# Optimization experiments

Hardware: AMD Instinct MI355X
Metric: run time of the kernel (lower is better)

Reference implementation:

```python
import jax, jax.numpy as jnp
import numpy as np

NS, B, T, S, H, V, G = 30, 16, 8, 400, 400, 20000, 3


def setup_inputs() -> dict:
    key = jax.random.key(0)
    ks = jax.random.split(key, 16)
    f = lambda k, shp, s: jax.random.normal(k, shp, jnp.float32) * s
    return dict(
        encoded_hidden=f(ks[0], (B, H), 1.0),
        encoded_outputs=f(ks[1], (B, S, H), 1.0),
        slot_emb=f(ks[2], (NS, H), 0.1),
        emb=f(ks[3], (V, H), 0.1),
        W_ih=f(ks[4], (3 * H, H), 0.05),
        W_hh=f(ks[5], (3 * H, H), 0.05),
        b_ih=jnp.zeros((3 * H,), jnp.float32),
        b_hh=jnp.zeros((3 * H,), jnp.float32),
        W_ratio_w=f(ks[6], (1, 3 * H), 0.05),
        W_ratio_b=jnp.zeros((1,), jnp.float32),
        W_gate_w=f(ks[7], (G, H), 0.05),
        W_gate_b=jnp.zeros((G,), jnp.float32),
        story=jax.random.randint(ks[8], (B, S), 0, V),
        target=jax.random.randint(ks[9], (B, NS, T), 0, V),
        encoded_lens=jax.random.randint(ks[10], (B,), S // 2, S + 1).astype(jnp.int32),
    )


def reference(encoded_hidden, encoded_outputs, slot_emb, emb, W_ih, W_hh, b_ih, b_hh,
              W_ratio_w, W_ratio_b, W_gate_w, W_gate_b, story, target, encoded_lens):
    ns, h = slot_emb.shape
    b, s, _ = encoded_outputs.shape
    t = target.shape[2]
    v = emb.shape[0]
    bs = ns * b  # fused slot*batch decode rows (parallel_decode)

    enc_out = jnp.tile(encoded_outputs, (ns, 1, 1))            # [bs,S,H]
    story_r = jnp.tile(story, (ns, 1))                          # [bs,S]
    lens_r = jnp.tile(encoded_lens, (ns,))                      # [bs]
    mask = jnp.arange(s)[None, :] < lens_r[:, None]             # [bs,S]
    h0 = jnp.tile(encoded_hidden, (ns, 1))                      # [bs,H]
    x0 = jnp.broadcast_to(slot_emb[:, None, :], (ns, b, h)).reshape(bs, h)
    # teacher-forcing inputs, slot-major flatten like target[:, :, wi].T.flatten()
    tf_in = emb[jnp.transpose(target, (2, 1, 0)).reshape(t, bs)]  # [T,bs,H]
    row = jnp.arange(bs)[:, None]
    neg_inf = jnp.float32(-jnp.inf)

    def gru_cell(x, hid):
        gi = x @ W_ih.T + b_ih
        gh = hid @ W_hh.T + b_hh
        ir, iz, inn = jnp.split(gi, 3, axis=-1)
        hr, hz, hn = jnp.split(gh, 3, axis=-1)
        r = jax.nn.sigmoid(ir + hr)
        z = jax.nn.sigmoid(iz + hz)
        n = jnp.tanh(inn + r * hn)
        return (1.0 - z) * n + z * hid

    def step(carry, x_next):
        hid, x = carry
        h_new = gru_cell(x, hid)                                # dec_state == hidden for 1-step GRU
        scores = jnp.einsum('bh,bsh->bs', h_new, enc_out)
        scores = jnp.where(mask, scores, neg_inf)
        prob = jax.nn.softmax(scores, axis=1)
        context = jnp.einsum('bs,bsh->bh', prob, enc_out)
        p_vocab = jax.nn.softmax(h_new @ emb.T, axis=1)         # [bs,V]
        p_gen_vec = jnp.concatenate([h_new, context, x], axis=-1)
        switch = jax.nn.sigmoid(p_gen_vec @ W_ratio_w.T + W_ratio_b)  # [bs,1]
        p_ctx = jnp.zeros((bs, v), p_vocab.dtype).at[row, story_r].add(prob)
        final = (1.0 - switch) * p_ctx + switch * p_vocab
        gate = context @ W_gate_w.T + W_gate_b
        return (h_new, x_next), (final, gate)

    _, (finals, gates) = jax.lax.scan(step, (h0, x0), tf_in)
    all_point = finals.reshape(t, ns, b, v).transpose(1, 2, 0, 3)  # [NS,B,T,V]
    all_gate = gates[0].reshape(ns, b, -1)                          # gates from wi==0
    return all_point, all_gate
```

## Files before the change

kernel.cpp:

```cpp
#include <hip/hip_runtime.h>
#include <hip/hip_bf16.h>

#define NSLOT 30
#define BB    16
#define TT    8
#define SS    400
#define HH    400
#define KP    416
#define NKK   13
#define VV    20000
#define GG    3
#define BSR   480
#define NBN   157
#define NCT   1256
#define NG2   1200
#define NCT2  75
#define NRT   30
#define FRAG_STRIDE 512

typedef unsigned short u16;
typedef __attribute__((ext_vector_type(8))) short bf16x8;
typedef __attribute__((ext_vector_type(4))) float f32x4;

__device__ __forceinline__ short f2bfs(float f){
  __hip_bfloat16 h = __float2bfloat16(f);
  union { __hip_bfloat16 b; short u; } v; v.b = h; return v.u;
}
__device__ __forceinline__ unsigned int pack2(float lo, float hi){
  return (unsigned int)(u16)f2bfs(lo) | ((unsigned int)(u16)f2bfs(hi) << 16);
}
__device__ __forceinline__ float bfu(u16 u){
  union { unsigned int i; float f; } v; v.i = ((unsigned int)u) << 16; return v.f;
}
__device__ __forceinline__ float bfu_lo(unsigned int u){
  union { unsigned int i; float f; } v; v.i = u << 16; return v.f;
}
__device__ __forceinline__ float bfu_hi(unsigned int u){
  union { unsigned int i; float f; } v; v.i = u & 0xffff0000u; return v.f;
}
__device__ __forceinline__ float sigm(float x){ return 1.f / (1.f + __expf(-x)); }
__device__ __forceinline__ float tanh_fast(float x){
  float e = __expf(2.f * x);
  return 1.f - 2.f / (e + 1.f);
}
__device__ __forceinline__ float wred_max(float v){
  #pragma unroll
  for (int off = 32; off; off >>= 1) v = fmaxf(v, __shfl_xor(v, off, 64));
  return v;
}
__device__ __forceinline__ float wred_sum(float v){
  #pragma unroll
  for (int off = 32; off; off >>= 1) v += __shfl_xor(v, off, 64);
  return v;
}

__global__ __launch_bounds__(256) void k_init_all(
    const float* __restrict__ eh, const float* __restrict__ semb,
    float* __restrict__ h_ws, float* __restrict__ x_ws,
    short* __restrict__ h_hi, short* __restrict__ h_lo,
    short* __restrict__ x_hi, short* __restrict__ x_lo)
{
  const int NU = NRT * NKK * 64;
  for (int u = blockIdx.x * 256 + threadIdx.x; u < 2 * NU; u += gridDim.x * 256){
    int uu = u; int sel = 0;
    if (uu >= NU){ uu -= NU; sel = 1; }
    short* ph = sel ? x_hi : h_hi;
    short* pl = sel ? x_lo : h_lo;
    float* fw = sel ? x_ws : h_ws;
    int lane = uu & 63, kt = uu >> 6;
    int rtile = kt / NKK, kk = kt - rtile * NKK;
    int lg = lane >> 4, rl = lane & 15;
    int r = rtile * 16 + rl, k = kk * 32 + lg * 8;
    const float* src = sel ? (semb + (size_t)rtile * HH)
                           : (eh   + (size_t)rl * HH);
    bf16x8 oh, ol;
    #pragma unroll
    for (int j = 0; j < 8; ++j){
      if (k + j < HH){
        float v = src[k + j];
        short hb = f2bfs(v);
        oh[j] = hb; ol[j] = f2bfs(v - bfu((u16)hb));
        fw[(size_t)r * HH + k + j] = v;
      } else { oh[j] = 0; ol[j] = 0; }
    }
    *reinterpret_cast<bf16x8*>(ph + (size_t)uu * 8) = oh;
    *reinterpret_cast<bf16x8*>(pl + (size_t)uu * 8) = ol;
  }
}

__global__ __launch_bounds__(256) void k_cast_W(
    const float* __restrict__ Wih, const float* __restrict__ Whh,
    short* __restrict__ Wih_hi, short* __restrict__ Wih_lo,
    short* __restrict__ Whh_hi, short* __restrict__ Whh_lo)
{
  const int NU = NCT2 * NKK * 64;
  for (int u = blockIdx.x * 256 + threadIdx.x; u < 2 * NU; u += gridDim.x * 256){
    int uu = u; int sel = 0;
    if (uu >= NU){ uu -= NU; sel = 1; }
    const float* W = sel ? Whh : Wih;
    short* ph = sel ? Whh_hi : Wih_hi;
    short* pl = sel ? Whh_lo : Wih_lo;
    int lane = uu & 63, kt = uu >> 6;
    int ctile = kt / NKK, kk = kt - ctile * NKK;
    int lg = lane >> 4, cl = lane & 15;
    int c = ctile * 16 + cl, k = kk * 32 + lg * 8;
    bf16x8 oh, ol;
    #pragma unroll
    for (int j = 0; j < 8; ++j){
      if (k + j < HH){
        float v = W[(size_t)c * HH + k + j];
        short hb = f2bfs(v);
        oh[j] = hb; ol[j] = f2bfs(v - bfu((u16)hb));
      } else { oh[j] = 0; ol[j] = 0; }
    }
    *reinterpret_cast<bf16x8*>(ph + (size_t)uu * 8) = oh;
    *reinterpret_cast<bf16x8*>(pl + (size_t)uu * 8) = ol;
  }
}

__global__ __launch_bounds__(256) void k_cast_emb(const float* __restrict__ emb,
                                                  short* __restrict__ ebf)
{
  const int nunit = NCT * NKK * 64;
  for (int u = blockIdx.x * 256 + threadIdx.x; u < nunit; u += gridDim.x * 256){
    int lane = u & 63;
    int kt = u >> 6;
    int ctile = kt / NKK, kk = kt - ctile * NKK;
    int lg = lane >> 4, cl = lane & 15;
    int c = ctile * 16 + cl;
    int k = kk * 32 + lg * 8;
    bf16x8 o;
    if (c < VV && k < HH){
      const float* src = emb + (size_t)c * HH + k;
      #pragma unroll
      for (int j = 0; j < 8; ++j) o[j] = f2bfs(src[j]);
    } else {
      #pragma unroll
      for (int j = 0; j < 8; ++j) o[j] = 0;
    }
    *reinterpret_cast<bf16x8*>(ebf + (size_t)u * 8) = o;
  }
}

__device__ __forceinline__ void gemm2_body(
    int bM, int bN, int z, int t,
    const short* __restrict__ x_hi, const short* __restrict__ x_lo,
    const short* __restrict__ h_hi, const short* __restrict__ h_lo,
    const short* __restrict__ Wih_hi, const short* __restrict__ Wih_lo,
    const short* __restrict__ Whh_hi, const short* __restrict__ Whh_lo,
    float* __restrict__ gi, float* __restrict__ gh)
{
  const int lane = t & 63, wid = t >> 6;
  const int wr = wid >> 1, wc = wid & 1;
  const int l15 = lane & 15, lg = lane >> 4;

  const short* A_hi = z ? h_hi : x_hi;
  const short* A_lo = z ? h_lo : x_lo;
  const short* B_hi = z ? Whh_hi : Wih_hi;
  const short* B_lo = z ? Whh_lo : Wih_lo;
  float* C = z ? gh : gi;

  const short *ah[4], *al[4], *bh[4], *bl[4];
  #pragma unroll
  for (int m = 0; m < 4; ++m){
    int rtile = min(bM * 8 + wr * 4 + m, NRT - 1);
    size_t off = (size_t)rtile * (NKK * FRAG_STRIDE) + lane * 8;
    ah[m] = A_hi + off; al[m] = A_lo + off;
  }
  #pragma unroll
  for (int n = 0; n < 4; ++n){
    int ctile = min(bN * 8 + wc * 4 + n, NCT2 - 1);
    size_t off = (size_t)ctile * (NKK * FRAG_STRIDE) + lane * 8;
    bh[n] = B_hi + off; bl[n] = B_lo + off;
  }

  f32x4 acc[4][4];
  #pragma unroll
  for (int m = 0; m < 4; ++m)
    #pragma unroll
    for (int n = 0; n < 4; ++n)
      acc[m][n] = (f32x4){0.f, 0.f, 0.f, 0.f};

  #pragma unroll
  for (int kk = 0; kk < NKK; ++kk){
    const int ko = kk * FRAG_STRIDE;
    bf16x8 ah_r[4], al_r[4];
    #pragma unroll
    for (int m = 0; m < 4; ++m){
      ah_r[m] = *reinterpret_cast<const bf16x8*>(ah[m] + ko);
      al_r[m] = *reinterpret_cast<const bf16x8*>(al[m] + ko);
    }
    #pragma unroll
    for (int n = 0; n < 4; ++n){
      bf16x8 bhv = *reinterpret_cast<const bf16x8*>(bh[n] + ko);
      bf16x8 blv = *reinterpret_cast<const bf16x8*>(bl[n] + ko);
      #pragma unroll
      for (int m = 0; m < 4; ++m){
        acc[m][n] = __builtin_amdgcn_mfma_f32_16x16x32_bf16(ah_r[m], bhv, acc[m][n], 0, 0, 0);
        acc[m][n] = __builtin_amdgcn_mfma_f32_16x16x32_bf16(ah_r[m], blv, acc[m][n], 0, 0, 0);
        acc[m][n] = __builtin_amdgcn_mfma_f32_16x16x32_bf16(al_r[m], bhv, acc[m][n], 0, 0, 0);
      }
    }
  }

  #pragma unroll
  for (int m = 0; m < 4; ++m){
    #pragma unroll
    for (int q = 0; q < 4; ++q){
      int row = bM * 128 + wr * 64 + m * 16 + lg * 4 + q;
      if (row < BSR){
        #pragma unroll
        for (int n = 0; n < 4; ++n){
          int col = bN * 128 + wc * 64 + n * 16 + l15;
          if (col < NG2) C[(size_t)row * NG2 + col] = acc[m][n][q];
        }
      }
    }
  }
}

__global__ __launch_bounds__(256) void k_gemm2_mfma(
    const short* __restrict__ x_hi, const short* __restrict__ x_lo,
    const short* __restrict__ h_hi, const short* __restrict__ h_lo,
    const short* __restrict__ Wih_hi, const short* __restrict__ Wih_lo,
    const short* __restrict__ Whh_hi, const short* __restrict__ Whh_lo,
    float* __restrict__ gi, float* __restrict__ gh)
{
  gemm2_body(blockIdx.x, blockIdx.y, blockIdx.z, threadIdx.x,
             x_hi, x_lo, h_hi, h_lo, Wih_hi, Wih_lo, Whh_hi, Whh_lo, gi, gh);
}

__global__ __launch_bounds__(256) void k_logits_mfma(
    const short* __restrict__ hbf, const short* __restrict__ ebf,
    float* __restrict__ out, float* __restrict__ pmax_ws,
    float* __restrict__ psum_ws, int wi)
{
  const int t = threadIdx.x;
  const int lane = t & 63, wid = t >> 6;
  const int wr = wid >> 1, wc = wid & 1;
  const int l15 = lane & 15, lg = lane >> 4;
  const int bM = blockIdx.x, bN = blockIdx.y;

  const short* ap[4];
  const short* bp[4];
  #pragma unroll
  for (int m = 0; m < 4; ++m){
    int rtile = bM * 8 + wr * 4 + m;
    ap[m] = hbf + (size_t)min(rtile, NRT - 1) * (NKK * FRAG_STRIDE) + lane * 8;
  }
  #pragma unroll
  for (int n = 0; n < 4; ++n){
    int ctile = bN * 8 + wc * 4 + n;
    bp[n] = ebf + (size_t)ctile * (NKK * FRAG_STRIDE) + lane * 8;
  }

  f32x4 acc[4][4];
  #pragma unroll
  for (int m = 0; m < 4; ++m)
    #pragma unroll
    for (int n = 0; n < 4; ++n)
      acc[m][n] = (f32x4){0.f, 0.f, 0.f, 0.f};

  #pragma unroll
  for (int kk = 0; kk < NKK; ++kk){
    const int ko = kk * FRAG_STRIDE;
    bf16x8 a[4];
    #pragma unroll
    for (int m = 0; m < 4; ++m)
      a[m] = *reinterpret_cast<const bf16x8*>(ap[m] + ko);
    #pragma unroll
    for (int n = 0; n < 4; ++n){
      bf16x8 b = *reinterpret_cast<const bf16x8*>(bp[n] + ko);
      #pragma unroll
      for (int m = 0; m < 4; ++m)
        acc[m][n] = __builtin_amdgcn_mfma_f32_16x16x32_bf16(a[m], b, acc[m][n], 0, 0, 0);
    }
  }

  #pragma unroll
  for (int m = 0; m < 4; ++m){
    #pragma unroll
    for (int q = 0; q < 4; ++q){
      int row = bM * 128 + wr * 64 + m * 16 + lg * 4 + q;
      u16* lrow16 = reinterpret_cast<u16*>(out + ((size_t)row * TT + wi) * VV);
      #pragma unroll
      for (int n = 0; n < 4; ++n){
        float v = acc[m][n][q];
        float vp = __shfl_xor(v, 1, 64);
        int col = bN * 128 + wc * 64 + n * 16 + l15;
        if (((l15 & 1) == 0) && row < BSR && col < VV)
          *reinterpret_cast<unsigned int*>(lrow16 + col) = pack2(v, vp);
      }
    }
    f32x4 rmax, rsum;
    #pragma unroll
    for (int q = 0; q < 4; ++q){
      float mx = -3.0e38f;
      #pragma unroll
      for (int n = 0; n < 4; ++n){
        int col = bN * 128 + wc * 64 + n * 16 + l15;
        float v = (col < VV) ? acc[m][n][q] : -3.0e38f;
        mx = fmaxf(mx, v);
      }
      #pragma unroll
      for (int off = 1; off < 16; off <<= 1) mx = fmaxf(mx, __shfl_xor(mx, off, 64));
      float sm = 0.f;
      #pragma unroll
      for (int n = 0; n < 4; ++n){
        int col = bN * 128 + wc * 64 + n * 16 + l15;
        if (col < VV) sm += __expf(acc[m][n][q] - mx);
      }
      #pragma unroll
      for (int off = 1; off < 16; off <<= 1) sm += __shfl_xor(sm, off, 64);
      rmax[q] = mx; rsum[q] = sm;
    }
    if (l15 == 0){
      #pragma unroll
      for (int q = 0; q < 4; ++q){
        int row = bM * 128 + wr * 64 + m * 16 + lg * 4 + q;
        if (row < BSR){
          size_t pidx = ((size_t)row * NBN + bN) * 2 + wc;
          pmax_ws[pidx] = rmax[q];
          psum_ws[pidx] = rsum[q];
        }
      }
    }
  }
}

__global__ __launch_bounds__(256) void k_att(
    const float* __restrict__ enc, const float* __restrict__ emb,
    const float* __restrict__ b_ih, const float* __restrict__ b_hh,
    const float* __restrict__ Wr_w, const float* __restrict__ Wr_b,
    const float* __restrict__ Wg_w, const float* __restrict__ Wg_b,
    const int* __restrict__ target, const int* __restrict__ lens,
    const float* __restrict__ gi_ws, const float* __restrict__ gh_ws,
    float* __restrict__ h_ws, float* __restrict__ x_ws,
    short* __restrict__ h_hi, short* __restrict__ h_lo,
    short* __restrict__ x_hi, short* __restrict__ x_lo,
    float* __restrict__ prob_ws, float* __restrict__ sw_ws,
    float* __restrict__ d_out, int wi)
{
  __shared__ float hn_s[HH];
  __shared__ float sc_s[SS];
  __shared__ float ctx_s[HH];
  __shared__ float red[4];
  __shared__ float redg[GG][4];

  const int t = threadIdx.x;
  const int rg = blockIdx.x;
  const int batch = rg % BB, slot = rg / BB;
  const int len = lens[batch];
  const int rtile = rg >> 4, rl = rg & 15;

  const float* gir = gi_ws + (size_t)rg * NG2;
  const float* ghr = gh_ws + (size_t)rg * NG2;
  for (int k = t; k < HH; k += 256){
    float irv = gir[k]          + b_ih[k];
    float izv = gir[HH + k]     + b_ih[HH + k];
    float inv = gir[2 * HH + k] + b_ih[2 * HH + k];
    float hrv = ghr[k]          + b_hh[k];
    float hzv = ghr[HH + k]     + b_hh[HH + k];
    float hnv = ghr[2 * HH + k] + b_hh[2 * HH + k];
    float rr = sigm(irv + hrv);
    float zz = sigm(izv + hzv);
    float nn = tanh_fast(inv + rr * hnv);
    float hold = h_ws[(size_t)rg * HH + k];
    float hnew = (1.f - zz) * nn + zz * hold;
    hn_s[k] = hnew;
    h_ws[(size_t)rg * HH + k] = hnew;
  }
  __syncthreads();

  if (t < KP / 8){
    const int kk = t >> 2, lg = t & 3;
    bf16x8 oh, ol;
    #pragma unroll
    for (int j = 0; j < 8; ++j){
      int k = t * 8 + j;
      if (k < HH){
        float v = hn_s[k];
        short hb = f2bfs(v);
        oh[j] = hb; ol[j] = f2bfs(v - bfu((u16)hb));
      } else { oh[j] = 0; ol[j] = 0; }
    }
    size_t off = ((size_t)rtile * NKK + kk) * FRAG_STRIDE + (lg * 16 + rl) * 8;
    *reinterpret_cast<bf16x8*>(h_hi + off) = oh;
    *reinterpret_cast<bf16x8*>(h_lo + off) = ol;
  }

  const float* encb = enc + (size_t)batch * SS * HH;
  float lmax = -3.0e38f;
  for (int s = t; s < SS; s += 256){
    if (s < len){
      const float4* er4 = reinterpret_cast<const float4*>(encb + (size_t)s * HH);
      float dot = 0.f;
      for (int k4 = 0; k4 < HH / 4; ++k4){
        float4 e = er4[k4];
        float4 hv = *reinterpret_cast<const float4*>(&hn_s[k4 * 4]);
        dot += e.x*hv.x + e.y*hv.y + e.z*hv.z + e.w*hv.w;
      }
      sc_s[s] = dot;
      lmax = fmaxf(lmax, dot);
    }
  }
  lmax = wred_max(lmax);
  if ((t & 63) == 0) red[t >> 6] = lmax;
  __syncthreads();
  lmax = fmaxf(fmaxf(red[0], red[1]), fmaxf(red[2], red[3]));
  float lsum = 0.f;
  for (int s = t; s < SS; s += 256){
    float e = (s < len) ? __expf(sc_s[s] - lmax) : 0.f;
    sc_s[s] = e;
    lsum += e;
  }
  lsum = wred_sum(lsum);
  __syncthreads();
  if ((t & 63) == 0) red[t >> 6] = lsum;
  __syncthreads();
  lsum = red[0] + red[1] + red[2] + red[3];
  float invl = 1.f / lsum;
  for (int s = t; s < SS; s += 256){
    float p = sc_s[s] * invl;
    sc_s[s] = p;
    prob_ws[(size_t)rg * SS + s] = p;
  }
  __syncthreads();

  for (int k = t; k < HH; k += 256){
    float c0 = 0.f, c1 = 0.f, c2 = 0.f, c3 = 0.f;
    const float* ek = encb + k;
    int s = 0;
    for (; s + 3 < len; s += 4){
      c0 += sc_s[s]     * ek[(size_t)s * HH];
      c1 += sc_s[s + 1] * ek[(size_t)(s + 1) * HH];
      c2 += sc_s[s + 2] * ek[(size_t)(s + 2) * HH];
      c3 += sc_s[s + 3] * ek[(size_t)(s + 3) * HH];
    }
    for (; s < len; ++s) c0 += sc_s[s] * ek[(size_t)s * HH];
    ctx_s[k] = (c0 + c1) + (c2 + c3);
  }
  __syncthreads();

  float sa = 0.f;
  for (int k = t; k < HH; k += 256){
    sa += Wr_w[k]          * hn_s[k]
        + Wr_w[HH + k]     * ctx_s[k]
        + Wr_w[2 * HH + k] * x_ws[(size_t)rg * HH + k];
  }
  sa = wred_sum(sa);
  if ((t & 63) == 0) red[t >> 6] = sa;
  __syncthreads();
  sa = red[0] + red[1] + red[2] + red[3];
  if (t == 0) sw_ws[rg] = sigm(sa + Wr_b[0]);

  if (wi == 0){
    float ga[GG] = {0.f, 0.f, 0.f};
    for (int k = t; k < HH; k += 256){
      float cv = ctx_s[k];
      ga[0] += Wg_w[k] * cv;
      ga[1] += Wg_w[HH + k] * cv;
      ga[2] += Wg_w[2 * HH + k] * cv;
    }
    #pragma unroll
    for (int g = 0; g < GG; ++g){
      ga[g] = wred_sum(ga[g]);
      if ((t & 63) == 0) redg[g][t >> 6] = ga[g];
    }
    __syncthreads();
    if (t < GG)
      d_out[(size_t)NSLOT * BB * TT * VV + (size_t)rg * GG + t] =
          redg[t][0] + redg[t][1] + redg[t][2] + redg[t][3] + Wg_b[t];
  }

  const int tgt = target[batch * (NSLOT * TT) + slot * TT + wi];
  const float* embrow = emb + (size_t)tgt * HH;
  for (int k = t; k < HH; k += 256)
    x_ws[(size_t)rg * HH + k] = embrow[k];
  if (t < KP / 8){
    const int kk = t >> 2, lg = t & 3;
    bf16x8 oh, ol;
    #pragma unroll
    for (int j = 0; j < 8; ++j){
      int k = t * 8 + j;
      if (k < HH){
        float v = embrow[k];
        short hb = f2bfs(v);
        oh[j] = hb; ol[j] = f2bfs(v - bfu((u16)hb));
      } else { oh[j] = 0; ol[j] = 0; }
    }
    size_t off = ((size_t)rtile * NKK + kk) * FRAG_STRIDE + (lg * 16 + rl) * 8;
    *reinterpret_cast<bf16x8*>(x_hi + off) = oh;
    *reinterpret_cast<bf16x8*>(x_lo + off) = ol;
  }
}

__global__ __launch_bounds__(256) void k_fin_gemm2(
    float* __restrict__ logits_out, const float* __restrict__ prob_ws,
    const float* __restrict__ pmax_ws, const float* __restrict__ psum_ws,
    const float* __restrict__ sw_ws, const int* __restrict__ story,
    const int* __restrict__ lens, int wi,
    const short* __restrict__ x_hi, const short* __restrict__ x_lo,
    const short* __restrict__ h_hi, const short* __restrict__ h_lo,
    const short* __restrict__ Wih_hi, const short* __restrict__ Wih_lo,
    const short* __restrict__ Whh_hi, const short* __restrict__ Whh_lo,
    float* __restrict__ gi, float* __restrict__ gh, int do_gemm)
{
  __shared__ float pctx[VV];
  __shared__ float red[4];
  const int t = threadIdx.x;

  if (blockIdx.x >= BSR){
    if (!do_gemm) return;
    int b = blockIdx.x - BSR;
    int bM = b & 3, bN = (b >> 2) % 10, z = b / 40;
    gemm2_body(bM, bN, z, t, x_hi, x_lo, h_hi, h_lo,
               Wih_hi, Wih_lo, Whh_hi, Whh_lo, gi, gh);
    return;
  }

  const int r = blockIdx.x;
  const int batch = r % BB;
  for (int v = t; v < VV; v += 256) pctx[v] = 0.f;
  __syncthreads();
  const int len = lens[batch];
  for (int s = t; s < SS; s += 256){
    if (s < len)
      atomicAdd(&pctx[story[batch * SS + s]], prob_ws[(size_t)r * SS + s]);
  }

  float* lrow = logits_out + ((size_t)r * TT + wi) * VV;
  const uint4* l16 = reinterpret_cast<const uint4*>(lrow);
  uint4 stage[10];
  {
    int ns = 0;
    for (int i = t; i < VV / 8; i += 256) stage[ns++] = l16[i];
  }

  const float* pm = pmax_ws + (size_t)r * (NBN * 2);
  const float* ps = psum_ws + (size_t)r * (NBN * 2);
  float m = -3.0e38f;
  for (int i = t; i < NBN * 2; i += 256) m = fmaxf(m, pm[i]);
  m = wred_max(m);
  if ((t & 63) == 0) red[t >> 6] = m;
  __syncthreads();
  m = fmaxf(fmaxf(red[0], red[1]), fmaxf(red[2], red[3]));
  float lsum = 0.f;
  for (int i = t; i < NBN * 2; i += 256) lsum += ps[i] * __expf(pm[i] - m);
  lsum = wred_sum(lsum);
  __syncthreads();
  if ((t & 63) == 0) red[t >> 6] = lsum;
  __syncthreads();
  lsum = red[0] + red[1] + red[2] + red[3];

  const float sw = sw_ws[r];
  const float invl = sw / lsum;
  const float osw = 1.f - sw;
  {
    int ns = 0;
    for (int i = t; i < VV / 8; i += 256){
      uint4 q = stage[ns++];
      int v = i * 8;
      float4 o0, o1;
      o0.x = __expf(bfu_lo(q.x) - m) * invl + osw * pctx[v + 0];
      o0.y = __expf(bfu_hi(q.x) - m) * invl + osw * pctx[v + 1];
      o0.z = __expf(bfu_lo(q.y) - m) * invl + osw * pctx[v + 2];
      o0.w = __expf(bfu_hi(q.y) - m) * invl + osw * pctx[v + 3];
      o1.x = __expf(bfu_lo(q.z) - m) * invl + osw * pctx[v + 4];
      o1.y = __expf(bfu_hi(q.z) - m) * invl + osw * pctx[v + 5];
      o1.z = __expf(bfu_lo(q.w) - m) * invl + osw * pctx[v + 6];
      o1.w = __expf(bfu_hi(q.w) - m) * invl + osw * pctx[v + 7];
      *reinterpret_cast<float4*>(lrow + v)     = o0;
      *reinterpret_cast<float4*>(lrow + v + 4) = o1;
    }
  }
}

extern "C" void kernel_launch(void* const* d_in, const int* in_sizes, int n_in,
                              void* d_out, int out_size, void* d_ws, size_t ws_size,
                              hipStream_t stream)
{
  (void)in_sizes; (void)n_in; (void)out_size; (void)ws_size;
  const float* eh    = (const float*)d_in[0];
  const float* enc   = (const float*)d_in[1];
  const float* semb  = (const float*)d_in[2];
  const float* emb   = (const float*)d_in[3];
  const float* W_ih  = (const float*)d_in[4];
  const float* W_hh  = (const float*)d_in[5];
  const float* b_ih  = (const float*)d_in[6];
  const float* b_hh  = (const float*)d_in[7];
  const float* Wr_w  = (const float*)d_in[8];
  const float* Wr_b  = (const float*)d_in[9];
  const float* Wg_w  = (const float*)d_in[10];
  const float* Wg_b  = (const float*)d_in[11];
  const int* story = (const int*)d_in[12];
  const int* tgt   = (const int*)d_in[13];
  const int* lens  = (const int*)d_in[14];
  float* out = (float*)d_out;

  float* ws      = (float*)d_ws;
  float* h_ws    = ws;
  float* x_ws    = ws + 192000;
  float* prob_ws = ws + 384000;
  float* sw_ws   = ws + 576000;
  float* gi_ws   = ws + 576512;
  float* gh_ws   = ws + 1152512;
  float* pmax_ws = ws + 1728512;
  float* psum_ws = ws + 1879552;
  short* h_hi    = (short*)(ws + 2030592);
  short* emb_bf  = (short*)(ws + 2130432);
  short* Wih_hi  = (short*)(ws + 6310400);
  short* Wih_lo  = (short*)(ws + 6560000);
  short* Whh_hi  = (short*)(ws + 6809600);
  short* Whh_lo  = (short*)(ws + 7059200);
  short* x_hi    = (short*)(ws + 7308800);
  short* x_lo    = (short*)(ws + 7408640);
  short* h_lo    = (short*)(ws + 7508480);

  k_cast_emb<<<2048, 256, 0, stream>>>(emb, emb_bf);
  k_cast_W<<<512, 256, 0, stream>>>(W_ih, W_hh, Wih_hi, Wih_lo, Whh_hi, Whh_lo);
  k_init_all<<<195, 256, 0, stream>>>(eh, semb, h_ws, x_ws,
                                      h_hi, h_lo, x_hi, x_lo);
  dim3 gg(4, 10, 2);
  k_gemm2_mfma<<<gg, 256, 0, stream>>>(x_hi, x_lo, h_hi, h_lo,
                                       Wih_hi, Wih_lo, Whh_hi, Whh_lo,
                                       gi_ws, gh_ws);
  for (int wi = 0; wi < TT; ++wi){
    k_att<<<BSR, 256, 0, stream>>>(enc, emb, b_ih, b_hh, Wr_w, Wr_b, Wg_w, Wg_b,
                                   tgt, lens, gi_ws, gh_ws, h_ws, x_ws,
                                   h_hi, h_lo, x_hi, x_lo,
                                   prob_ws, sw_ws, out, wi);
    dim3 gl(4, NBN);
    k_logits_mfma<<<gl, 256, 0, stream>>>(h_hi, emb_bf, out, pmax_ws, psum_ws, wi);
    k_fin_gemm2<<<BSR + 80, 256, 0, stream>>>(out, prob_ws, pmax_ws, psum_ws,
                                              sw_ws, story, lens, wi,
                                              x_hi, x_lo, h_hi, h_lo,
                                              Wih_hi, Wih_lo, Whh_hi, Whh_lo,
                                              gi_ws, gh_ws, (wi + 1 < TT) ? 1 : 0);
  }
}
```

Measured before the change: 974.9 us.

## Split GRU update into own kernel and co-schedule attention with logits GEMM

```diff
diff --git a/kernel.cpp b/kernel.cpp
--- a/kernel.cpp
+++ b/kernel.cpp
@@ -230,132 +230,20 @@
              x_hi, x_lo, h_hi, h_lo, Wih_hi, Wih_lo, Whh_hi, Whh_lo, gi, gh);
 }
 
-__global__ __launch_bounds__(256) void k_logits_mfma(
-    const short* __restrict__ hbf, const short* __restrict__ ebf,
-    float* __restrict__ out, float* __restrict__ pmax_ws,
-    float* __restrict__ psum_ws, int wi)
-{
-  const int t = threadIdx.x;
-  const int lane = t & 63, wid = t >> 6;
-  const int wr = wid >> 1, wc = wid & 1;
-  const int l15 = lane & 15, lg = lane >> 4;
-  const int bM = blockIdx.x, bN = blockIdx.y;
-
-  const short* ap[4];
-  const short* bp[4];
-  #pragma unroll
-  for (int m = 0; m < 4; ++m){
-    int rtile = bM * 8 + wr * 4 + m;
-    ap[m] = hbf + (size_t)min(rtile, NRT - 1) * (NKK * FRAG_STRIDE) + lane * 8;
-  }
-  #pragma unroll
-  for (int n = 0; n < 4; ++n){
-    int ctile = bN * 8 + wc * 4 + n;
-    bp[n] = ebf + (size_t)ctile * (NKK * FRAG_STRIDE) + lane * 8;
-  }
-
-  f32x4 acc[4][4];
-  #pragma unroll
-  for (int m = 0; m < 4; ++m)
-    #pragma unroll
-    for (int n = 0; n < 4; ++n)
-      acc[m][n] = (f32x4){0.f, 0.f, 0.f, 0.f};
-
-  #pragma unroll
-  for (int kk = 0; kk < NKK; ++kk){
-    const int ko = kk * FRAG_STRIDE;
-    bf16x8 a[4];
-    #pragma unroll
-    for (int m = 0; m < 4; ++m)
-      a[m] = *reinterpret_cast<const bf16x8*>(ap[m] + ko);
-    #pragma unroll
-    for (int n = 0; n < 4; ++n){
-      bf16x8 b = *reinterpret_cast<const bf16x8*>(bp[n] + ko);
-      #pragma unroll
-      for (int m = 0; m < 4; ++m)
-        acc[m][n] = __builtin_amdgcn_mfma_f32_16x16x32_bf16(a[m], b, acc[m][n], 0, 0, 0);
-    }
-  }
-
-  #pragma unroll
-  for (int m = 0; m < 4; ++m){
-    #pragma unroll
-    for (int q = 0; q < 4; ++q){
-      int row = bM * 128 + wr * 64 + m * 16 + lg * 4 + q;
-      u16* lrow16 = reinterpret_cast<u16*>(out + ((size_t)row * TT + wi) * VV);
-      #pragma unroll
-      for (int n = 0; n < 4; ++n){
-        float v = acc[m][n][q];
-        float vp = __shfl_xor(v, 1, 64);
-        int col = bN * 128 + wc * 64 + n * 16 + l15;
-        if (((l15 & 1) == 0) && row < BSR && col < VV)
-          *reinterpret_cast<unsigned int*>(lrow16 + col) = pack2(v, vp);
-      }
-    }
-    f32x4 rmax, rsum;
-    #pragma unroll
-    for (int q = 0; q < 4; ++q){
-      float mx = -3.0e38f;
-      #pragma unroll
-      for (int n = 0; n < 4; ++n){
-        int col = bN * 128 + wc * 64 + n * 16 + l15;
-        float v = (col < VV) ? acc[m][n][q] : -3.0e38f;
-        mx = fmaxf(mx, v);
-      }
-      #pragma unroll
-      for (int off = 1; off < 16; off <<= 1) mx = fmaxf(mx, __shfl_xor(mx, off, 64));
-      float sm = 0.f;
-      #pragma unroll
-      for (int n = 0; n < 4; ++n){
-        int col = bN * 128 + wc * 64 + n * 16 + l15;
-        if (col < VV) sm += __expf(acc[m][n][q] - mx);
-      }
-      #pragma unroll
-      for (int off = 1; off < 16; off <<= 1) sm += __shfl_xor(sm, off, 64);
-      rmax[q] = mx; rsum[q] = sm;
-    }
-    if (l15 == 0){
-      #pragma unroll
-      for (int q = 0; q < 4; ++q){
-        int row = bM * 128 + wr * 64 + m * 16 + lg * 4 + q;
-        if (row < BSR){
-          size_t pidx = ((size_t)row * NBN + bN) * 2 + wc;
-          pmax_ws[pidx] = rmax[q];
-          psum_ws[pidx] = rsum[q];
-        }
-      }
-    }
-  }
-}
-
-__global__ __launch_bounds__(256) void k_att(
-    const float* __restrict__ enc, const float* __restrict__ emb,
+__global__ __launch_bounds__(128) void k_gru(
+    const float* __restrict__ gi_ws, const float* __restrict__ gh_ws,
     const float* __restrict__ b_ih, const float* __restrict__ b_hh,
-    const float* __restrict__ Wr_w, const float* __restrict__ Wr_b,
-    const float* __restrict__ Wg_w, const float* __restrict__ Wg_b,
-    const int* __restrict__ target, const int* __restrict__ lens,
-    const float* __restrict__ gi_ws, const float* __restrict__ gh_ws,
-    float* __restrict__ h_ws, float* __restrict__ x_ws,
-    short* __restrict__ h_hi, short* __restrict__ h_lo,
-    short* __restrict__ x_hi, short* __restrict__ x_lo,
-    float* __restrict__ prob_ws, float* __restrict__ sw_ws,
-    float* __restrict__ d_out, int wi)
+    float* __restrict__ h_ws,
+    short* __restrict__ h_hi, short* __restrict__ h_lo)
 {
   __shared__ float hn_s[HH];
-  __shared__ float sc_s[SS];
-  __shared__ float ctx_s[HH];
-  __shared__ float red[4];
-  __shared__ float redg[GG][4];
-
   const int t = threadIdx.x;
   const int rg = blockIdx.x;
-  const int batch = rg % BB, slot = rg / BB;
-  const int len = lens[batch];
   const int rtile = rg >> 4, rl = rg & 15;
 
   const float* gir = gi_ws + (size_t)rg * NG2;
   const float* ghr = gh_ws + (size_t)rg * NG2;
-  for (int k = t; k < HH; k += 256){
+  for (int k = t; k < HH; k += 128){
     float irv = gir[k]          + b_ih[k];
     float izv = gir[HH + k]     + b_ih[HH + k];
     float inv = gir[2 * HH + k] + b_ih[2 * HH + k];
@@ -388,18 +276,153 @@
     *reinterpret_cast<bf16x8*>(h_hi + off) = oh;
     *reinterpret_cast<bf16x8*>(h_lo + off) = ol;
   }
+}
+
+__device__ __forceinline__ void logits_body(
+    int bM, int bN, int t,
+    const short* __restrict__ hbf, const short* __restrict__ ebf,
+    float* __restrict__ out, float* __restrict__ pmax_ws,
+    float* __restrict__ psum_ws, int wi)
+{
+  const int lane = t & 63, wid = t >> 6;
+  const int wr = wid >> 1, wc = wid & 1;
+  const int l15 = lane & 15, lg = lane >> 4;
+
+  const short* ap[4];
+  const short* bp[4];
+  #pragma unroll
+  for (int m = 0; m < 4; ++m){
+    int rtile = bM * 8 + wr * 4 + m;
+    ap[m] = hbf + (size_t)min(rtile, NRT - 1) * (NKK * FRAG_STRIDE) + lane * 8;
+  }
+  #pragma unroll
+  for (int n = 0; n < 4; ++n){
+    int ctile = bN * 8 + wc * 4 + n;
+    bp[n] = ebf + (size_t)ctile * (NKK * FRAG_STRIDE) + lane * 8;
+  }
+
+  f32x4 acc[4][4];
+  #pragma unroll
+  for (int m = 0; m < 4; ++m)
+    #pragma unroll
+    for (int n = 0; n < 4; ++n)
+      acc[m][n] = (f32x4){0.f, 0.f, 0.f, 0.f};
+
+  #pragma unroll
+  for (int kk = 0; kk < NKK; ++kk){
+    const int ko = kk * FRAG_STRIDE;
+    bf16x8 a[4];
+    #pragma unroll
+    for (int m = 0; m < 4; ++m)
+      a[m] = *reinterpret_cast<const bf16x8*>(ap[m] + ko);
+    #pragma unroll
+    for (int n = 0; n < 4; ++n){
+      bf16x8 b = *reinterpret_cast<const bf16x8*>(bp[n] + ko);
+      #pragma unroll
+      for (int m = 0; m < 4; ++m)
+        acc[m][n] = __builtin_amdgcn_mfma_f32_16x16x32_bf16(a[m], b, acc[m][n], 0, 0, 0);
+    }
+  }
+
+  #pragma unroll
+  for (int m = 0; m < 4; ++m){
+    #pragma unroll
+    for (int q = 0; q < 4; ++q){
+      int row = bM * 128 + wr * 64 + m * 16 + lg * 4 + q;
+      u16* lrow16 = reinterpret_cast<u16*>(out + ((size_t)row * TT + wi) * VV);
+      #pragma unroll
+      for (int n = 0; n < 4; ++n){
+        float v = acc[m][n][q];
+        float vp = __shfl_xor(v, 1, 64);
+        int col = bN * 128 + wc * 64 + n * 16 + l15;
+        if (((l15 & 1) == 0) && row < BSR && col < VV)
+          *reinterpret_cast<unsigned int*>(lrow16 + col) = pack2(v, vp);
+      }
+    }
+    f32x4 rmax, rsum;
+    #pragma unroll
+    for (int q = 0; q < 4; ++q){
+      float mx = -3.0e38f;
+      #pragma unroll
+      for (int n = 0; n < 4; ++n){
+        int col = bN * 128 + wc * 64 + n * 16 + l15;
+        float v = (col < VV) ? acc[m][n][q] : -3.0e38f;
+        mx = fmaxf(mx, v);
+      }
+      #pragma unroll
+      for (int off = 1; off < 16; off <<= 1) mx = fmaxf(mx, __shfl_xor(mx, off, 64));
+      float sm = 0.f;
+      #pragma unroll
+      for (int n = 0; n < 4; ++n){
+        int col = bN * 128 + wc * 64 + n * 16 + l15;
+        if (col < VV) sm += __expf(acc[m][n][q] - mx);
+      }
+      #pragma unroll
+      for (int off = 1; off < 16; off <<= 1) sm += __shfl_xor(sm, off, 64);
+      rmax[q] = mx; rsum[q] = sm;
+    }
+    if (l15 == 0){
+      #pragma unroll
+      for (int q = 0; q < 4; ++q){
+        int row = bM * 128 + wr * 64 + m * 16 + lg * 4 + q;
+        if (row < BSR){
+          size_t pidx = ((size_t)row * NBN + bN) * 2 + wc;
+          pmax_ws[pidx] = rmax[q];
+          psum_ws[pidx] = rsum[q];
+        }
+      }
+    }
+  }
+}
+
+__global__ __launch_bounds__(256) void k_att_logits(
+    const float* __restrict__ enc, const float* __restrict__ emb,
+    const float* __restrict__ Wr_w, const float* __restrict__ Wr_b,
+    const float* __restrict__ Wg_w, const float* __restrict__ Wg_b,
+    const int* __restrict__ target, const int* __restrict__ lens,
+    const float* __restrict__ h_ws, float* __restrict__ x_ws,
+    short* __restrict__ x_hi, short* __restrict__ x_lo,
+    float* __restrict__ prob_ws, float* __restrict__ sw_ws,
+    const short* __restrict__ h_hi, const short* __restrict__ ebf,
+    float* __restrict__ d_out, float* __restrict__ pmax_ws,
+    float* __restrict__ psum_ws, int wi)
+{
+  __shared__ float hn_s[HH];
+  __shared__ float sc_s[SS];
+  __shared__ float ctx_s[HH];
+  __shared__ float red[4];
+  __shared__ float redg[GG][4];
+
+  const int t = threadIdx.x;
+
+  if (blockIdx.x >= BSR){
+    int b = blockIdx.x - BSR;
+    logits_body(b & 3, b >> 2, t, h_hi, ebf, d_out, pmax_ws, psum_ws, wi);
+    return;
+  }
+
+  const int rg = blockIdx.x;
+  const int batch = rg % BB, slot = rg / BB;
+  const int len = lens[batch];
+  const int rtile = rg >> 4, rl = rg & 15;
+
+  for (int k = t; k < HH; k += 256) hn_s[k] = h_ws[(size_t)rg * HH + k];
+  __syncthreads();
 
   const float* encb = enc + (size_t)batch * SS * HH;
   float lmax = -3.0e38f;
   for (int s = t; s < SS; s += 256){
     if (s < len){
       const float4* er4 = reinterpret_cast<const float4*>(encb + (size_t)s * HH);
-      float dot = 0.f;
-      for (int k4 = 0; k4 < HH / 4; ++k4){
-        float4 e = er4[k4];
-        float4 hv = *reinterpret_cast<const float4*>(&hn_s[k4 * 4]);
-        dot += e.x*hv.x + e.y*hv.y + e.z*hv.z + e.w*hv.w;
+      float d0 = 0.f, d1 = 0.f;
+      for (int k4 = 0; k4 < HH / 4; k4 += 2){
+        float4 e0 = er4[k4], e1 = er4[k4 + 1];
+        float4 h0 = *reinterpret_cast<const float4*>(&hn_s[k4 * 4]);
+        float4 h1 = *reinterpret_cast<const float4*>(&hn_s[k4 * 4 + 4]);
+        d0 += e0.x*h0.x + e0.y*h0.y + e0.z*h0.z + e0.w*h0.w;
+        d1 += e1.x*h1.x + e1.y*h1.y + e1.z*h1.z + e1.w*h1.w;
       }
+      float dot = d0 + d1;
       sc_s[s] = dot;
       lmax = fmaxf(lmax, dot);
     }
@@ -626,12 +649,10 @@
                                        Wih_hi, Wih_lo, Whh_hi, Whh_lo,
                                        gi_ws, gh_ws);
   for (int wi = 0; wi < TT; ++wi){
-    k_att<<<BSR, 256, 0, stream>>>(enc, emb, b_ih, b_hh, Wr_w, Wr_b, Wg_w, Wg_b,
-                                   tgt, lens, gi_ws, gh_ws, h_ws, x_ws,
-                                   h_hi, h_lo, x_hi, x_lo,
-                                   prob_ws, sw_ws, out, wi);
-    dim3 gl(4, NBN);
-    k_logits_mfma<<<gl, 256, 0, stream>>>(h_hi, emb_bf, out, pmax_ws, psum_ws, wi);
+    k_gru<<<BSR, 128, 0, stream>>>(gi_ws, gh_ws, b_ih, b_hh, h_ws, h_hi, h_lo);
+    k_att_logits<<<BSR + 4 * NBN, 256, 0, stream>>>(
+        enc, emb, Wr_w, Wr_b, Wg_w, Wg_b, tgt, lens, h_ws, x_ws,
+        x_hi, x_lo, prob_ws, sw_ws, h_hi, emb_bf, out, pmax_ws, psum_ws, wi);
     k_fin_gemm2<<<BSR + 80, 256, 0, stream>>>(out, prob_ws, pmax_ws, psum_ws,
                                               sw_ws, story, lens, wi,
                                               x_hi, x_lo, h_hi, h_lo,
```

Result: slower. 1.051 ms (+7.8%).
